# Kernel tuning notes

Hardware: AMD Instinct MI355X
Metric: run time of the kernel (lower is better)

The kernel has to match this reference:

```python
import jax, jax.numpy as jnp
import numpy as np

LAYERS = 5      # lstm_layers
H = 1           # lstm_hidden_size
IN = 21         # 9 (rot) + 6 (v) + 6 (u)
NEG = 0.1       # LeakyReLU negative slope
EPS = 1e-5      # BatchNorm1d eps


def _lstm_cell(x, h, c, w_ih, w_hh):
    # torch gate order: i, f, g, o ; no biases (lstm_bias=False)
    gates = x @ w_ih.T + h @ w_hh.T              # [k, 4H]
    i, f, g, o = jnp.split(gates, 4, axis=-1)
    i = jax.nn.sigmoid(i)
    f = jax.nn.sigmoid(f)
    g = jnp.tanh(g)
    o = jax.nn.sigmoid(o)
    c_new = f * c + i * g
    h_new = o * jnp.tanh(c_new)
    return h_new, c_new


def _bn_train(z, gamma, beta):
    # BatchNorm1d in training mode: batch stats, biased variance
    m = z.mean(axis=0)
    var = z.var(axis=0)
    return gamma * (z - m) / jnp.sqrt(var + EPS) + beta


def setup_inputs() -> dict:
    key = jax.random.key(0)
    ks = jax.random.split(key, 14)
    k, T = 65536, 32
    s = 0.2  # init scale, roughly torch uniform(-1/sqrt(H)) magnitude
    inp = {
        "r": jax.random.normal(ks[0], (k, T, 9), jnp.float32),
        "v": jax.random.normal(ks[1], (k, T, 6), jnp.float32),
        "u": jax.random.normal(ks[2], (k, T, 6), jnp.float32),
        # LSTM weights: layer 0 sees IN features, layers 1..4 see H
        "w_ih0": jax.random.normal(ks[3], (4 * H, IN), jnp.float32) * s,
        "w_ih_rest": jax.random.normal(ks[4], (LAYERS - 1, 4 * H, H), jnp.float32) * s,
        "w_hh": jax.random.normal(ks[5], (LAYERS, 4 * H, H), jnp.float32) * s,
        # FC head: Linear(H,32,no bias) -> BN -> LReLU -> Linear(32,32) -> BN -> LReLU -> Linear(32,6)
        "W1": jax.random.normal(ks[6], (32, H), jnp.float32) * s,
        "g1": jnp.ones((32,), jnp.float32),
        "b1": jnp.zeros((32,), jnp.float32),
        "W2": jax.random.normal(ks[7], (32, 32), jnp.float32) * s,
        "g2": jnp.ones((32,), jnp.float32),
        "b2": jnp.zeros((32,), jnp.float32),
        "W3": jax.random.normal(ks[8], (6, 32), jnp.float32) * s,
    }
    return inp


def reference(r, v, u, w_ih0, w_ih_rest, w_hh, W1, g1, b1, W2, g2, b2, W3):
    x = jnp.concatenate([r, v, u], axis=-1)          # [k, T, 21]
    k = x.shape[0]
    h0 = jnp.zeros((LAYERS, k, H), x.dtype)
    c0 = jnp.zeros((LAYERS, k, H), x.dtype)
    xs = jnp.swapaxes(x, 0, 1)                       # [T, k, 21]

    def step(carry, xt):
        h, c = carry
        hs, cs = [], []
        layer_in = xt
        for l in range(LAYERS):
            w_ih = w_ih0 if l == 0 else w_ih_rest[l - 1]
            hl, cl = _lstm_cell(layer_in, h[l], c[l], w_ih, w_hh[l])
            hs.append(hl)
            cs.append(cl)
            layer_in = hl
        return (jnp.stack(hs), jnp.stack(cs)), layer_in  # top-layer output

    (hT, cT), outs = jax.lax.scan(step, (h0, c0), xs)    # outs: [T, k, H]

    # fc applied to out[:, 0] -> first timestep of top layer
    y = outs[0]                                          # [k, H]
    y = jax.nn.leaky_relu(_bn_train(y @ W1.T, g1, b1), NEG)
    y = jax.nn.leaky_relu(_bn_train(y @ W2.T, g2, b2), NEG)
    dv = y @ W3.T                                        # [k, 6]
    return dv[:, None], hT, cT
```

## Files before the change

kernel.cpp:

```cpp
#include <hip/hip_runtime.h>
#include <math.h>

#define T 32
#define NEGS 0.1f
#define EPS 1e-5f
#define NREG 33


__device__ __forceinline__ float rcp_fast(float x) { return __builtin_amdgcn_rcpf(x); }
__device__ __forceinline__ float sigm(float x) { return rcp_fast(1.0f + __expf(-x)); }
__device__ __forceinline__ float tanh_fast(float x) {
    float t = __expf(2.0f * fabsf(x));
    float r = 1.0f - 2.0f * rcp_fast(t + 1.0f);
    return copysignf(r, x);
}
__device__ __forceinline__ float lrelu(float x) { return x > 0.0f ? x : NEGS * x; }

__device__ __forceinline__ void bn1_params(const float* __restrict__ W1,
                                           const float* __restrict__ g1,
                                           const float* __restrict__ b1,
                                           const double* __restrict__ wsd, int k, int j,
                                           float& my, float& vy, float& a, float& b,
                                           float& tau, int& flip)
{
    my = (float)(wsd[0] / k);
    vy = (float)(wsd[1] / k) - my * my;
    float wj = W1[j];
    a = g1[j] * wj * rsqrtf(fmaf(wj * wj, vy, EPS));
    b = b1[j];
    if (a > 0.0f)      { tau = my - b / a; flip = 0; }
    else if (a < 0.0f) { tau = my - b / a; flip = 1; }
    else               { tau = (b > 0.0f ? -__builtin_inff() : __builtin_inff()); flip = 0; }
}

__global__ __launch_bounds__(256)
void gates_kernel(const float* __restrict__ r, const float* __restrict__ v,
                  const float* __restrict__ u, const float* __restrict__ wih0,
                  float4* __restrict__ xg, int k, int ngroups)
{
    __shared__ float rbuf[8 * 32 * 9];
    __shared__ float vbuf[8 * 32 * 6];
    __shared__ float ubuf[8 * 32 * 6];
    __shared__ float obuf[32 * 36];
    const int tid = threadIdx.x;

    float4* rb4 = reinterpret_cast<float4*>(rbuf);
    float4* vb4 = reinterpret_cast<float4*>(vbuf);
    float4* ub4 = reinterpret_cast<float4*>(ubuf);

    float wi0[4][21];
#pragma unroll
    for (int g = 0; g < 4; ++g)
#pragma unroll
        for (int j = 0; j < 21; ++j) wi0[g][j] = wih0[g * 21 + j];

    float4 Ra0, Ra1, Ra2, Rv0, Rv1, Ru0, Ru1;

#define ISSUE_GROUP(gg)                                                         \
    do {                                                                        \
        const float4* r4_ = reinterpret_cast<const float4*>(r + (size_t)(gg) * (8 * T * 9)); \
        const float4* v4_ = reinterpret_cast<const float4*>(v + (size_t)(gg) * (8 * T * 6)); \
        const float4* u4_ = reinterpret_cast<const float4*>(u + (size_t)(gg) * (8 * T * 6)); \
        Ra0 = r4_[tid];                                                         \
        Ra1 = r4_[256 + tid];                                                   \
        if (tid < 64) Ra2 = r4_[512 + tid];                                     \
        Rv0 = v4_[tid];                                                         \
        if (tid < 128) Rv1 = v4_[256 + tid];                                    \
        Ru0 = u4_[tid];                                                         \
        if (tid < 128) Ru1 = u4_[256 + tid];                                    \
    } while (0)

    int g = blockIdx.x;
    const int gstride = gridDim.x;
    if (g >= ngroups) return;
    ISSUE_GROUP(g);

    while (g < ngroups) {
        rb4[tid] = Ra0;
        rb4[256 + tid] = Ra1;
        if (tid < 64) rb4[512 + tid] = Ra2;
        vb4[tid] = Rv0;
        if (tid < 128) vb4[256 + tid] = Rv1;
        ub4[tid] = Ru0;
        if (tid < 128) ub4[256 + tid] = Ru1;

        const int gn = g + gstride;
        if (gn < ngroups) ISSUE_GROUP(gn);

        __syncthreads();

        const int sl = tid >> 5, t = tid & 31;
        float x[21];
#pragma unroll
        for (int j = 0; j < 9; ++j) x[j] = rbuf[sl * (32 * 9) + t * 9 + j];
#pragma unroll
        for (int j = 0; j < 6; ++j) x[9 + j] = vbuf[sl * (32 * 6) + t * 6 + j];
#pragma unroll
        for (int j = 0; j < 6; ++j) x[15 + j] = ubuf[sl * (32 * 6) + t * 6 + j];

        float4 g4;
        float* gp = (float*)&g4;
#pragma unroll
        for (int gi = 0; gi < 4; ++gi) {
            float acc = 0.f;
#pragma unroll
            for (int j = 0; j < 21; ++j) acc = fmaf(wi0[gi][j], x[j], acc);
            gp[gi] = acc;
        }
        *(float4*)&obuf[t * 36 + sl * 4] = g4;
        __syncthreads();

        const int tG = tid >> 3, j = tid & 7;
        float4 val = *(const float4*)&obuf[tG * 36 + j * 4];
        xg[(size_t)tG * k + g * 8 + j] = val;

        g = gn;
    }
#undef ISSUE_GROUP
}

__global__ __launch_bounds__(256, 1)
void recur_kernel(const float4* __restrict__ xg, const float* __restrict__ wihr,
                  const float* __restrict__ whhp, float* __restrict__ out,
                  double* __restrict__ wsd, float* __restrict__ wsy, int k)
{
    const int s = blockIdx.x * 256 + threadIdx.x;

    float4 gbuf[T];
#pragma unroll
    for (int t = 0; t < T; ++t) gbuf[t] = xg[(size_t)t * k + s];

    float wir[4][4];
#pragma unroll
    for (int l = 0; l < 4; ++l)
#pragma unroll
        for (int g = 0; g < 4; ++g) wir[l][g] = wihr[l * 4 + g];
    float whh[5][4];
#pragma unroll
    for (int l = 0; l < 5; ++l)
#pragma unroll
        for (int g = 0; g < 4; ++g) whh[l][g] = whhp[l * 4 + g];

    asm volatile("" ::: "memory");

    float h[5] = {0.f, 0.f, 0.f, 0.f, 0.f};
    float c[5] = {0.f, 0.f, 0.f, 0.f, 0.f};
    float y0 = 0.f;

#pragma unroll
    for (int t = 0; t < T; ++t) {
        const float4 G = gbuf[t];
        float a0 = fmaf(whh[0][0], h[0], G.x);
        float a1 = fmaf(whh[0][1], h[0], G.y);
        float a2 = fmaf(whh[0][2], h[0], G.z);
        float a3 = fmaf(whh[0][3], h[0], G.w);
        {
            float ii = sigm(a0), ff = sigm(a1);
            float gg = tanh_fast(a2), oo = sigm(a3);
            c[0] = ff * c[0] + ii * gg;
            h[0] = oo * tanh_fast(c[0]);
        }
        float xin = h[0];
#pragma unroll
        for (int l = 1; l < 5; ++l) {
            float b0 = fmaf(wir[l - 1][0], xin, whh[l][0] * h[l]);
            float b1 = fmaf(wir[l - 1][1], xin, whh[l][1] * h[l]);
            float b2 = fmaf(wir[l - 1][2], xin, whh[l][2] * h[l]);
            float b3 = fmaf(wir[l - 1][3], xin, whh[l][3] * h[l]);
            float ii = sigm(b0), ff = sigm(b1);
            float gg = tanh_fast(b2), oo = sigm(b3);
            c[l] = ff * c[l] + ii * gg;
            h[l] = oo * tanh_fast(c[l]);
            xin = h[l];
        }
        if (t == 0) y0 = h[4];
    }

#pragma unroll
    for (int l = 0; l < 5; ++l) {
        out[(size_t)6 * k + (size_t)l * k + s] = h[l];
        out[(size_t)11 * k + (size_t)l * k + s] = c[l];
    }
    wsy[s] = y0;

    float ys = y0, yq = y0 * y0;
#pragma unroll
    for (int off = 32; off; off >>= 1) {
        ys += __shfl_down(ys, off);
        yq += __shfl_down(yq, off);
    }
    __shared__ float pS[4], pQ[4];
    const int wid = threadIdx.x >> 6, lane = threadIdx.x & 63;
    if (lane == 0) { pS[wid] = ys; pQ[wid] = yq; }
    __syncthreads();
    if (threadIdx.x == 0) {
        atomicAdd(&wsd[0], (double)(pS[0] + pS[1] + pS[2] + pS[3]));
        atomicAdd(&wsd[1], (double)(pQ[0] + pQ[1] + pQ[2] + pQ[3]));
    }
}

__global__ __launch_bounds__(256, 1)
void lstm_fused(const float* __restrict__ r, const float* __restrict__ v,
                const float* __restrict__ u,
                const float* __restrict__ wih0, const float* __restrict__ wihr,
                const float* __restrict__ whhp,
                float* __restrict__ out, double* __restrict__ wsd,
                float* __restrict__ wsy, int k)
{
    const int s = blockIdx.x * 256 + threadIdx.x;
    float wi0[4][21];
#pragma unroll
    for (int g = 0; g < 4; ++g)
#pragma unroll
        for (int j = 0; j < 21; ++j) wi0[g][j] = wih0[g * 21 + j];
    float wir[4][4];
#pragma unroll
    for (int l = 0; l < 4; ++l)
#pragma unroll
        for (int g = 0; g < 4; ++g) wir[l][g] = wihr[l * 4 + g];
    float whh[5][4];
#pragma unroll
    for (int l = 0; l < 5; ++l)
#pragma unroll
        for (int g = 0; g < 4; ++g) whh[l][g] = whhp[l * 4 + g];

    const float4* r4 = reinterpret_cast<const float4*>(r + (size_t)s * (T * 9));
    const float4* v4 = reinterpret_cast<const float4*>(v + (size_t)s * (T * 6));
    const float4* u4 = reinterpret_cast<const float4*>(u + (size_t)s * (T * 6));

    float h[5] = {0.f, 0.f, 0.f, 0.f, 0.f};
    float c[5] = {0.f, 0.f, 0.f, 0.f, 0.f};
    float y0 = 0.f;

    for (int t0 = 0; t0 < T; t0 += 4) {
        const int cb = t0 >> 2;
        float4 rb[9], vb[6], ub[6];
#pragma unroll
        for (int q = 0; q < 9; ++q) rb[q] = r4[cb * 9 + q];
#pragma unroll
        for (int q = 0; q < 6; ++q) vb[q] = v4[cb * 6 + q];
#pragma unroll
        for (int q = 0; q < 6; ++q) ub[q] = u4[cb * 6 + q];
        float rf[36], vf[24], uf[24];
#pragma unroll
        for (int q = 0; q < 9; ++q) {
            rf[4 * q] = rb[q].x; rf[4 * q + 1] = rb[q].y;
            rf[4 * q + 2] = rb[q].z; rf[4 * q + 3] = rb[q].w;
        }
#pragma unroll
        for (int q = 0; q < 6; ++q) {
            vf[4 * q] = vb[q].x; vf[4 * q + 1] = vb[q].y;
            vf[4 * q + 2] = vb[q].z; vf[4 * q + 3] = vb[q].w;
            uf[4 * q] = ub[q].x; uf[4 * q + 1] = ub[q].y;
            uf[4 * q + 2] = ub[q].z; uf[4 * q + 3] = ub[q].w;
        }
#pragma unroll
        for (int dt = 0; dt < 4; ++dt) {
            float x[21];
#pragma unroll
            for (int j = 0; j < 9; ++j) x[j] = rf[dt * 9 + j];
#pragma unroll
            for (int j = 0; j < 6; ++j) x[9 + j] = vf[dt * 6 + j];
#pragma unroll
            for (int j = 0; j < 6; ++j) x[15 + j] = uf[dt * 6 + j];
            float gt[4];
#pragma unroll
            for (int g = 0; g < 4; ++g) {
                float a = whh[0][g] * h[0];
#pragma unroll
                for (int j = 0; j < 21; ++j) a = fmaf(wi0[g][j], x[j], a);
                gt[g] = a;
            }
            {
                float ii = sigm(gt[0]), ff = sigm(gt[1]);
                float gg = tanh_fast(gt[2]), oo = sigm(gt[3]);
                c[0] = ff * c[0] + ii * gg;
                h[0] = oo * tanh_fast(c[0]);
            }
            float xin = h[0];
#pragma unroll
            for (int l = 1; l < 5; ++l) {
                float b0 = fmaf(wir[l - 1][0], xin, whh[l][0] * h[l]);
                float b1 = fmaf(wir[l - 1][1], xin, whh[l][1] * h[l]);
                float b2 = fmaf(wir[l - 1][2], xin, whh[l][2] * h[l]);
                float b3 = fmaf(wir[l - 1][3], xin, whh[l][3] * h[l]);
                float ii = sigm(b0), ff = sigm(b1);
                float gg = tanh_fast(b2), oo = sigm(b3);
                c[l] = ff * c[l] + ii * gg;
                h[l] = oo * tanh_fast(c[l]);
                xin = h[l];
            }
            if (t0 + dt == 0) y0 = h[4];
        }
    }
#pragma unroll
    for (int l = 0; l < 5; ++l) {
        out[(size_t)6 * k + (size_t)l * k + s] = h[l];
        out[(size_t)11 * k + (size_t)l * k + s] = c[l];
    }
    wsy[s] = y0;
    float ys = y0, yq = y0 * y0;
#pragma unroll
    for (int off = 32; off; off >>= 1) {
        ys += __shfl_down(ys, off);
        yq += __shfl_down(yq, off);
    }
    __shared__ float pS[4], pQ[4];
    const int wid = threadIdx.x >> 6, lane = threadIdx.x & 63;
    if (lane == 0) { pS[wid] = ys; pQ[wid] = yq; }
    __syncthreads();
    if (threadIdx.x == 0) {
        atomicAdd(&wsd[0], (double)(pS[0] + pS[1] + pS[2] + pS[3]));
        atomicAdd(&wsd[1], (double)(pQ[0] + pQ[1] + pQ[2] + pQ[3]));
    }
}

__global__ __launch_bounds__(256)
void hist_kernel(const float* __restrict__ W1, const float* __restrict__ g1,
                 const float* __restrict__ b1, double* __restrict__ wsd,
                 const float* __restrict__ wsy, int k)
{
    __shared__ float sTau[32];
    __shared__ float sH[3 * NREG];
    __shared__ float sMy;
    const int tid = threadIdx.x;
    if (tid < 3 * NREG) sH[tid] = 0.f;
    if (tid < 32) {
        float my, vy, a, b, tau; int flip;
        bn1_params(W1, g1, b1, wsd, k, tid, my, vy, a, b, tau, flip);
        sTau[tid] = tau;
        if (tid == 0) sMy = my;
    }
    __syncthreads();
    const int stride = gridDim.x * 256;
    for (int s = blockIdx.x * 256 + tid; s < k; s += stride) {
        const float y = wsy[s];
        const float yc = y - sMy;
        int rgn = 0;
#pragma unroll
        for (int j = 0; j < 32; ++j) rgn += (y > sTau[j]) ? 1 : 0;
        atomicAdd(&sH[rgn], 1.0f);
        atomicAdd(&sH[NREG + rgn], yc);
        atomicAdd(&sH[2 * NREG + rgn], yc * yc);
    }
    __syncthreads();
    if (tid < 3 * NREG) atomicAdd(&wsd[2 + tid], (double)sH[tid]);
}

__global__ __launch_bounds__(256)
void tables_kernel(const float* __restrict__ W1, const float* __restrict__ g1,
                   const float* __restrict__ b1, const float* __restrict__ W2,
                   const float* __restrict__ g2, const float* __restrict__ b2,
                   const double* __restrict__ wsd, float* __restrict__ gPQ, int k)
{
    __shared__ float sA[32], sB[32], sTau[32];
    __shared__ int sRank[32], sFlip[32];
    __shared__ float sS0[NREG], sS1[NREG], sS2[NREG];
    __shared__ float sW2[1024];
    __shared__ float sSumY1[32];
    __shared__ float sM[1024];
    __shared__ float sI2[32], sM2v[32], sB2[32];
    const int tid = threadIdx.x;

    for (int i = tid; i < 1024; i += 256) sW2[i] = W2[i];
    if (tid < NREG) {
        sS0[tid] = (float)wsd[2 + tid];
        sS1[tid] = (float)wsd[2 + NREG + tid];
        sS2[tid] = (float)wsd[2 + 2 * NREG + tid];
    }
    if (tid < 32) {
        float my, vy, a, b, tau; int flip;
        bn1_params(W1, g1, b1, wsd, k, tid, my, vy, a, b, tau, flip);
        sA[tid] = a; sB[tid] = b; sTau[tid] = tau; sFlip[tid] = flip;
        sB2[tid] = b2[tid];
    }
    __syncthreads();
    if (tid < 32) {
        int rk = 0;
        float tj = sTau[tid];
#pragma unroll
        for (int l = 0; l < 32; ++l)
            rk += (sTau[l] < tj || (sTau[l] == tj && l < tid)) ? 1 : 0;
        sRank[tid] = rk;
    }
    __syncthreads();
    if (tid < 32) {
        const int rk = sRank[tid], fl = sFlip[tid];
        const float a = sA[tid], b = sB[tid];
        float acc = 0.f;
        for (int rg = 0; rg < NREG; ++rg) {
            float m = (((rk < rg) ? 1 : 0) != fl) ? 1.0f : NEGS;
            acc += m * (a * sS1[rg] + b * sS0[rg]);
        }
        sSumY1[tid] = acc;
    }
    for (int p = tid; p < 1024; p += 256) {
        const int j = p >> 5, l = p & 31;
        const int rj = sRank[j], fj = sFlip[j];
        const int rl = sRank[l], flp = sFlip[l];
        const float aj = sA[j], bj = sB[j], al = sA[l], bl = sB[l];
        const float caa = aj * al, cab = aj * bl + al * bj, cbb = bj * bl;
        float acc = 0.f;
        for (int rg = 0; rg < NREG; ++rg) {
            float mj = (((rj < rg) ? 1 : 0) != fj) ? 1.0f : NEGS;
            float ml = (((rl < rg) ? 1 : 0) != flp) ? 1.0f : NEGS;
            acc += mj * ml * (caa * sS2[rg] + cab * sS1[rg] + cbb * sS0[rg]);
        }
        sM[p] = acc;
    }
    __syncthreads();
    if (tid < 32) {
        const int i = tid;
        float s2 = 0.f, ss2 = 0.f;
#pragma unroll
        for (int j = 0; j < 32; ++j) {
            float wij = sW2[i * 32 + j];
            s2 = fmaf(wij, sSumY1[j], s2);
            float tj = 0.f;
#pragma unroll
            for (int l = 0; l < 32; ++l) tj = fmaf(sW2[i * 32 + l], sM[j * 32 + l], tj);
            ss2 = fmaf(wij, tj, ss2);
        }
        float m2 = s2 / k;
        float v2 = ss2 / k - m2 * m2;
        sM2v[i] = m2;
        sI2[i] = g2[i] * rsqrtf(v2 + EPS);
    }
    __syncthreads();
    for (int idx = tid; idx < NREG * 32; idx += 256) {
        const int rg = idx >> 5, i = idx & 31;
        float Ai = 0.f, Bi = 0.f;
#pragma unroll
        for (int j = 0; j < 32; ++j) {
            float m = (((sRank[j] < rg) ? 1 : 0) != sFlip[j]) ? 1.0f : NEGS;
            float w = sW2[i * 32 + j] * m;
            Ai = fmaf(w, sA[j], Ai);
            Bi = fmaf(w, sB[j], Bi);
        }
        gPQ[idx] = sI2[i] * Ai;
        gPQ[NREG * 32 + idx] = sI2[i] * (Bi - sM2v[i]) + sB2[i];
    }
}

__global__ __launch_bounds__(256)
void final_kernel(const float* __restrict__ W1, const float* __restrict__ g1,
                  const float* __restrict__ b1, const float* __restrict__ W3,
                  const double* __restrict__ wsd, const float* __restrict__ wsy,
                  const float* __restrict__ gPQ, float* __restrict__ out, int k)
{
    __shared__ float sTau[32], sW3[192], sMy;
    __shared__ float sP[NREG][33], sQ[NREG][33];
    const int tid = threadIdx.x;
    for (int idx = tid; idx < NREG * 32; idx += 256) {
        const int rg = idx >> 5, i = idx & 31;
        sP[rg][i] = gPQ[idx];
        sQ[rg][i] = gPQ[NREG * 32 + idx];
    }
    if (tid < 192) sW3[tid] = W3[tid];
    if (tid < 32) {
        float my, vy, a, b, tau; int flip;
        bn1_params(W1, g1, b1, wsd, k, tid, my, vy, a, b, tau, flip);
        sTau[tid] = tau;
        if (tid == 0) sMy = my;
    }
    __syncthreads();
    const int s = blockIdx.x * 256 + tid;
    const float y = wsy[s];
    const float yc = y - sMy;
    int rgn = 0;
#pragma unroll
    for (int j = 0; j < 32; ++j) rgn += (y > sTau[j]) ? 1 : 0;
    float dv[6] = {0.f, 0.f, 0.f, 0.f, 0.f, 0.f};
#pragma unroll
    for (int i = 0; i < 32; ++i) {
        float y2 = lrelu(fmaf(sP[rgn][i], yc, sQ[rgn][i]));
#pragma unroll
        for (int m = 0; m < 6; ++m) dv[m] = fmaf(sW3[m * 32 + i], y2, dv[m]);
    }
#pragma unroll
    for (int m = 0; m < 6; ++m) out[(size_t)s * 6 + m] = dv[m];
}

extern "C" void kernel_launch(void* const* d_in, const int* in_sizes, int n_in,
                              void* d_out, int out_size, void* d_ws, size_t ws_size,
                              hipStream_t stream)
{
    const float* r    = (const float*)d_in[0];
    const float* v    = (const float*)d_in[1];
    const float* u    = (const float*)d_in[2];
    const float* wih0 = (const float*)d_in[3];
    const float* wihr = (const float*)d_in[4];
    const float* whhp = (const float*)d_in[5];
    const float* W1   = (const float*)d_in[6];
    const float* g1v  = (const float*)d_in[7];
    const float* b1v  = (const float*)d_in[8];
    const float* W2   = (const float*)d_in[9];
    const float* g2v  = (const float*)d_in[10];
    const float* b2v  = (const float*)d_in[11];
    const float* W3   = (const float*)d_in[12];

    const int k = in_sizes[0] / (T * 9);
    float* out = (float*)d_out;
    double* wsd = (double*)d_ws;
    float* wsy = (float*)((char*)d_ws + 1024);

    const size_t xg_off = 1024 + (size_t)k * 4;
    const size_t need = xg_off + (size_t)k * T * 16 + (size_t)NREG * 32 * 2 * 4;

    hipMemsetAsync(d_ws, 0, 1024, stream);

    const int blocks = k / 256;
    float* gPQ;
    if (ws_size >= need) {
        float4* xg = (float4*)((char*)d_ws + xg_off);
        gPQ = (float*)((char*)d_ws + xg_off + (size_t)k * T * 16);
        const int ngroups = k / 8;
        int pblocks = 1536;
        if (pblocks > ngroups) pblocks = ngroups;
        gates_kernel<<<pblocks, 256, 0, stream>>>(r, v, u, wih0, xg, k, ngroups);
        recur_kernel<<<blocks, 256, 0, stream>>>(xg, wihr, whhp, out, wsd, wsy, k);
    } else {
        gPQ = (float*)((char*)d_ws + xg_off);
        lstm_fused<<<blocks, 256, 0, stream>>>(r, v, u, wih0, wihr, whhp, out, wsd, wsy, k);
    }
    hist_kernel<<<64, 256, 0, stream>>>(W1, g1v, b1v, wsd, wsy, k);
    tables_kernel<<<1, 256, 0, stream>>>(W1, g1v, b1v, W2, g2v, b2v, wsd, gPQ, k);
    final_kernel<<<blocks, 256, 0, stream>>>(W1, g1v, b1v, W3, wsd, wsy, gPQ, out, k);
}
```

Measured before the change: 266.6 us.

## Fuse input-gate projection into recurrence kernel via shared-memory handoff

The separate gates kernel and recurrence kernel are merged into one. Each block loads its 256 sequences in 32 cooperative groups of 8, computes the layer-0 input projections, and hands each thread its 32 gate vectors through shared memory instead of a global xg buffer. This removes the 32 MB intermediate write and read and one kernel launch. The cost is that the projection phase is serialised within each block, with two barriers per group, and there is one block per CU with heavy register use from the 32 float4 gate buffer.

```diff
diff --git a/kernel.cpp b/kernel.cpp
--- a/kernel.cpp
+++ b/kernel.cpp
@@ -33,16 +33,19 @@
     else               { tau = (b > 0.0f ? -__builtin_inff() : __builtin_inff()); flip = 0; }
 }
 
-__global__ __launch_bounds__(256)
-void gates_kernel(const float* __restrict__ r, const float* __restrict__ v,
+__global__ __launch_bounds__(256, 1)
+void fused_kernel(const float* __restrict__ r, const float* __restrict__ v,
                   const float* __restrict__ u, const float* __restrict__ wih0,
-                  float4* __restrict__ xg, int k, int ngroups)
+                  const float* __restrict__ wihr, const float* __restrict__ whhp,
+                  float* __restrict__ out, double* __restrict__ wsd,
+                  float* __restrict__ wsy, int k)
 {
     __shared__ float rbuf[8 * 32 * 9];
     __shared__ float vbuf[8 * 32 * 6];
     __shared__ float ubuf[8 * 32 * 6];
-    __shared__ float obuf[32 * 36];
+    __shared__ float4 pbuf[32][9];
     const int tid = threadIdx.x;
+    const int sBase = blockIdx.x * 256;
 
     float4* rb4 = reinterpret_cast<float4*>(rbuf);
     float4* vb4 = reinterpret_cast<float4*>(vbuf);
@@ -53,14 +56,27 @@
     for (int g = 0; g < 4; ++g)
 #pragma unroll
         for (int j = 0; j < 21; ++j) wi0[g][j] = wih0[g * 21 + j];
+    float wir[4][4];
+#pragma unroll
+    for (int l = 0; l < 4; ++l)
+#pragma unroll
+        for (int g = 0; g < 4; ++g) wir[l][g] = wihr[l * 4 + g];
+    float whh[5][4];
+#pragma unroll
+    for (int l = 0; l < 5; ++l)
+#pragma unroll
+        for (int g = 0; g < 4; ++g) whh[l][g] = whhp[l * 4 + g];
+
+    float4 gbuf[T];
 
     float4 Ra0, Ra1, Ra2, Rv0, Rv1, Ru0, Ru1;
 
 #define ISSUE_GROUP(gg)                                                         \
     do {                                                                        \
-        const float4* r4_ = reinterpret_cast<const float4*>(r + (size_t)(gg) * (8 * T * 9)); \
-        const float4* v4_ = reinterpret_cast<const float4*>(v + (size_t)(gg) * (8 * T * 6)); \
-        const float4* u4_ = reinterpret_cast<const float4*>(u + (size_t)(gg) * (8 * T * 6)); \
+        const int s0_ = sBase + (gg) * 8;                                       \
+        const float4* r4_ = reinterpret_cast<const float4*>(r + (size_t)s0_ * (T * 9)); \
+        const float4* v4_ = reinterpret_cast<const float4*>(v + (size_t)s0_ * (T * 6)); \
+        const float4* u4_ = reinterpret_cast<const float4*>(u + (size_t)s0_ * (T * 6)); \
         Ra0 = r4_[tid];                                                         \
         Ra1 = r4_[256 + tid];                                                   \
         if (tid < 64) Ra2 = r4_[512 + tid];                                     \
@@ -70,12 +86,9 @@
         if (tid < 128) Ru1 = u4_[256 + tid];                                    \
     } while (0)
 
-    int g = blockIdx.x;
-    const int gstride = gridDim.x;
-    if (g >= ngroups) return;
-    ISSUE_GROUP(g);
-
-    while (g < ngroups) {
+    ISSUE_GROUP(0);
+
+    for (int sg = 0; sg < 32; ++sg) {
         rb4[tid] = Ra0;
         rb4[256 + tid] = Ra1;
         if (tid < 64) rb4[512 + tid] = Ra2;
@@ -84,8 +97,7 @@
         ub4[tid] = Ru0;
         if (tid < 128) ub4[256 + tid] = Ru1;
 
-        const int gn = g + gstride;
-        if (gn < ngroups) ISSUE_GROUP(gn);
+        if (sg < 31) ISSUE_GROUP(sg + 1);
 
         __syncthreads();
 
@@ -107,42 +119,18 @@
             for (int j = 0; j < 21; ++j) acc = fmaf(wi0[gi][j], x[j], acc);
             gp[gi] = acc;
         }
-        *(float4*)&obuf[t * 36 + sl * 4] = g4;
+        pbuf[t][sl] = g4;
         __syncthreads();
 
-        const int tG = tid >> 3, j = tid & 7;
-        float4 val = *(const float4*)&obuf[tG * 36 + j * 4];
-        xg[(size_t)tG * k + g * 8 + j] = val;
-
-        g = gn;
+        if ((tid >> 3) == sg) {
+            const int l = tid & 7;
+#pragma unroll
+            for (int tt = 0; tt < T; ++tt) gbuf[tt] = pbuf[tt][l];
+        }
     }
 #undef ISSUE_GROUP
-}
-
-__global__ __launch_bounds__(256, 1)
-void recur_kernel(const float4* __restrict__ xg, const float* __restrict__ wihr,
-                  const float* __restrict__ whhp, float* __restrict__ out,
-                  double* __restrict__ wsd, float* __restrict__ wsy, int k)
-{
-    const int s = blockIdx.x * 256 + threadIdx.x;
-
-    float4 gbuf[T];
-#pragma unroll
-    for (int t = 0; t < T; ++t) gbuf[t] = xg[(size_t)t * k + s];
-
-    float wir[4][4];
-#pragma unroll
-    for (int l = 0; l < 4; ++l)
-#pragma unroll
-        for (int g = 0; g < 4; ++g) wir[l][g] = wihr[l * 4 + g];
-    float whh[5][4];
-#pragma unroll
-    for (int l = 0; l < 5; ++l)
-#pragma unroll
-        for (int g = 0; g < 4; ++g) whh[l][g] = whhp[l * 4 + g];
-
-    asm volatile("" ::: "memory");
-
+
+    const int s = sBase + tid;
     float h[5] = {0.f, 0.f, 0.f, 0.f, 0.f};
     float c[5] = {0.f, 0.f, 0.f, 0.f, 0.f};
     float y0 = 0.f;
@@ -183,122 +171,6 @@
     }
     wsy[s] = y0;
 
-    float ys = y0, yq = y0 * y0;
-#pragma unroll
-    for (int off = 32; off; off >>= 1) {
-        ys += __shfl_down(ys, off);
-        yq += __shfl_down(yq, off);
-    }
-    __shared__ float pS[4], pQ[4];
-    const int wid = threadIdx.x >> 6, lane = threadIdx.x & 63;
-    if (lane == 0) { pS[wid] = ys; pQ[wid] = yq; }
-    __syncthreads();
-    if (threadIdx.x == 0) {
-        atomicAdd(&wsd[0], (double)(pS[0] + pS[1] + pS[2] + pS[3]));
-        atomicAdd(&wsd[1], (double)(pQ[0] + pQ[1] + pQ[2] + pQ[3]));
-    }
-}
-
-__global__ __launch_bounds__(256, 1)
-void lstm_fused(const float* __restrict__ r, const float* __restrict__ v,
-                const float* __restrict__ u,
-                const float* __restrict__ wih0, const float* __restrict__ wihr,
-                const float* __restrict__ whhp,
-                float* __restrict__ out, double* __restrict__ wsd,
-                float* __restrict__ wsy, int k)
-{
-    const int s = blockIdx.x * 256 + threadIdx.x;
-    float wi0[4][21];
-#pragma unroll
-    for (int g = 0; g < 4; ++g)
-#pragma unroll
-        for (int j = 0; j < 21; ++j) wi0[g][j] = wih0[g * 21 + j];
-    float wir[4][4];
-#pragma unroll
-    for (int l = 0; l < 4; ++l)
-#pragma unroll
-        for (int g = 0; g < 4; ++g) wir[l][g] = wihr[l * 4 + g];
-    float whh[5][4];
-#pragma unroll
-    for (int l = 0; l < 5; ++l)
-#pragma unroll
-        for (int g = 0; g < 4; ++g) whh[l][g] = whhp[l * 4 + g];
-
-    const float4* r4 = reinterpret_cast<const float4*>(r + (size_t)s * (T * 9));
-    const float4* v4 = reinterpret_cast<const float4*>(v + (size_t)s * (T * 6));
-    const float4* u4 = reinterpret_cast<const float4*>(u + (size_t)s * (T * 6));
-
-    float h[5] = {0.f, 0.f, 0.f, 0.f, 0.f};
-    float c[5] = {0.f, 0.f, 0.f, 0.f, 0.f};
-    float y0 = 0.f;
-
-    for (int t0 = 0; t0 < T; t0 += 4) {
-        const int cb = t0 >> 2;
-        float4 rb[9], vb[6], ub[6];
-#pragma unroll
-        for (int q = 0; q < 9; ++q) rb[q] = r4[cb * 9 + q];
-#pragma unroll
-        for (int q = 0; q < 6; ++q) vb[q] = v4[cb * 6 + q];
-#pragma unroll
-        for (int q = 0; q < 6; ++q) ub[q] = u4[cb * 6 + q];
-        float rf[36], vf[24], uf[24];
-#pragma unroll
-        for (int q = 0; q < 9; ++q) {
-            rf[4 * q] = rb[q].x; rf[4 * q + 1] = rb[q].y;
-            rf[4 * q + 2] = rb[q].z; rf[4 * q + 3] = rb[q].w;
-        }
-#pragma unroll
-        for (int q = 0; q < 6; ++q) {
-            vf[4 * q] = vb[q].x; vf[4 * q + 1] = vb[q].y;
-            vf[4 * q + 2] = vb[q].z; vf[4 * q + 3] = vb[q].w;
-            uf[4 * q] = ub[q].x; uf[4 * q + 1] = ub[q].y;
-            uf[4 * q + 2] = ub[q].z; uf[4 * q + 3] = ub[q].w;
-        }
-#pragma unroll
-        for (int dt = 0; dt < 4; ++dt) {
-            float x[21];
-#pragma unroll
-            for (int j = 0; j < 9; ++j) x[j] = rf[dt * 9 + j];
-#pragma unroll
-            for (int j = 0; j < 6; ++j) x[9 + j] = vf[dt * 6 + j];
-#pragma unroll
-            for (int j = 0; j < 6; ++j) x[15 + j] = uf[dt * 6 + j];
-            float gt[4];
-#pragma unroll
-            for (int g = 0; g < 4; ++g) {
-                float a = whh[0][g] * h[0];
-#pragma unroll
-                for (int j = 0; j < 21; ++j) a = fmaf(wi0[g][j], x[j], a);
-                gt[g] = a;
-            }
-            {
-                float ii = sigm(gt[0]), ff = sigm(gt[1]);
-                float gg = tanh_fast(gt[2]), oo = sigm(gt[3]);
-                c[0] = ff * c[0] + ii * gg;
-                h[0] = oo * tanh_fast(c[0]);
-            }
-            float xin = h[0];
-#pragma unroll
-            for (int l = 1; l < 5; ++l) {
-                float b0 = fmaf(wir[l - 1][0], xin, whh[l][0] * h[l]);
-                float b1 = fmaf(wir[l - 1][1], xin, whh[l][1] * h[l]);
-                float b2 = fmaf(wir[l - 1][2], xin, whh[l][2] * h[l]);
-                float b3 = fmaf(wir[l - 1][3], xin, whh[l][3] * h[l]);
-                float ii = sigm(b0), ff = sigm(b1);
-                float gg = tanh_fast(b2), oo = sigm(b3);
-                c[l] = ff * c[l] + ii * gg;
-                h[l] = oo * tanh_fast(c[l]);
-                xin = h[l];
-            }
-            if (t0 + dt == 0) y0 = h[4];
-        }
-    }
-#pragma unroll
-    for (int l = 0; l < 5; ++l) {
-        out[(size_t)6 * k + (size_t)l * k + s] = h[l];
-        out[(size_t)11 * k + (size_t)l * k + s] = c[l];
-    }
-    wsy[s] = y0;
     float ys = y0, yq = y0 * y0;
 #pragma unroll
     for (int off = 32; off; off >>= 1) {
@@ -503,26 +375,13 @@
     float* out = (float*)d_out;
     double* wsd = (double*)d_ws;
     float* wsy = (float*)((char*)d_ws + 1024);
-
-    const size_t xg_off = 1024 + (size_t)k * 4;
-    const size_t need = xg_off + (size_t)k * T * 16 + (size_t)NREG * 32 * 2 * 4;
+    float* gPQ = (float*)((char*)d_ws + 1024 + (size_t)k * 4);
 
     hipMemsetAsync(d_ws, 0, 1024, stream);
 
     const int blocks = k / 256;
-    float* gPQ;
-    if (ws_size >= need) {
-        float4* xg = (float4*)((char*)d_ws + xg_off);
-        gPQ = (float*)((char*)d_ws + xg_off + (size_t)k * T * 16);
-        const int ngroups = k / 8;
-        int pblocks = 1536;
-        if (pblocks > ngroups) pblocks = ngroups;
-        gates_kernel<<<pblocks, 256, 0, stream>>>(r, v, u, wih0, xg, k, ngroups);
-        recur_kernel<<<blocks, 256, 0, stream>>>(xg, wihr, whhp, out, wsd, wsy, k);
-    } else {
-        gPQ = (float*)((char*)d_ws + xg_off);
-        lstm_fused<<<blocks, 256, 0, stream>>>(r, v, u, wih0, wihr, whhp, out, wsd, wsy, k);
-    }
+    fused_kernel<<<blocks, 256, 0, stream>>>(r, v, u, wih0, wihr, whhp,
+                                             out, wsd, wsy, k);
     hist_kernel<<<64, 256, 0, stream>>>(W1, g1v, b1v, wsd, wsy, k);
     tables_kernel<<<1, 256, 0, stream>>>(W1, g1v, b1v, W2, g2v, b2v, wsd, gPQ, k);
     final_kernel<<<blocks, 256, 0, stream>>>(W1, g1v, b1v, W3, wsd, wsy, gPQ, out, k);
```

Result: no change. 262.7 us (-1.5%).
